# Optimization experiments

Measured on AMD Instinct MI355X. Metric: run time of the kernel, lower is better.

Reference implementation:

```python
import jax, jax.numpy as jnp
import numpy as np

B, S, D_MODEL = 4, 2048, 1024
N_HEADS, D_HEAD = 16, 64
HIDDEN = N_HEADS * D_HEAD
N_PRIM, RANK = 16, 256
CHUNK = 64  # matches CHUNK_SIZE in the torch module


def setup_inputs() -> dict:
    key = jax.random.key(0)
    ks = jax.random.split(key, 16)
    def n(k, shape, scale=0.02):
        return jax.random.normal(k, shape, dtype=jnp.float32) * scale
    return {
        'x': jax.random.normal(ks[0], (B, S, D_MODEL), dtype=jnp.float32),
        'q_U': n(ks[1], (N_PRIM, D_MODEL, RANK)),
        'q_V': n(ks[2], (N_PRIM, RANK, HIDDEN)),
        'k_U': n(ks[3], (N_PRIM, D_MODEL, RANK)),
        'k_V': n(ks[4], (N_PRIM, RANK, HIDDEN)),
        'v_U': n(ks[5], (N_PRIM, D_MODEL, RANK)),
        'v_V': n(ks[6], (N_PRIM, RANK, HIDDEN)),
        'q_logits': jax.random.normal(ks[7], (N_PRIM,), dtype=jnp.float32),
        'k_logits': jax.random.normal(ks[8], (N_PRIM,), dtype=jnp.float32),
        'v_logits': jax.random.normal(ks[9], (N_PRIM,), dtype=jnp.float32),
        'gate_logits': jax.random.normal(ks[10], (N_PRIM,), dtype=jnp.float32),
        'decay_w': n(ks[11], (N_HEADS, D_MODEL), 0.03),
        'decay_b': jnp.full((N_HEADS,), -2.0, dtype=jnp.float32),
        'out_gate_w': n(ks[12], (HIDDEN, D_MODEL), 0.03),
        'out_proj_w': n(ks[13], (D_MODEL, HIDDEN), 0.03),
        'rms_w': jnp.ones((HIDDEN,), dtype=jnp.float32),
        'top_k': 4,
    }


def _bank_topk_fused(x, U, V, logits, top_k):
    """Top-k fused mixture of low-rank primitives: sum_j w_j * (x @ U_j @ V_j)."""
    w = jax.nn.softmax(logits)                      # [P]
    vals, idx = jax.lax.top_k(w, top_k)             # [k], [k]
    vals = vals / jnp.sum(vals)                     # renormalize selected weights
    Us = U[idx]                                     # [k, d_in, rank]
    Vs = V[idx]                                     # [k, rank, d_out]
    h = jnp.einsum('bsd,kdr->bskr', x, Us)          # low-rank bottleneck
    return jnp.einsum('bskr,kro,k->bso', h, Vs, vals)


def _chunked_scan(q, kv, log_decay):
    """Decay-gated linear recurrence via chunked parallel scan (CHUNK=64).
    q, kv: [B,S,H,D]; log_decay: [B,S,H,1]. Returns [B,S,H,D]."""
    b, s, h, d = q.shape
    nc = s // CHUNK
    # [NC, B, C, H, *] chunked layout for lax.scan over chunks
    qc = jnp.moveaxis(q.reshape(b, nc, CHUNK, h, d), 1, 0)
    kvc = jnp.moveaxis(kv.reshape(b, nc, CHUNK, h, d), 1, 0)
    ldc = jnp.moveaxis(log_decay.reshape(b, nc, CHUNK, h, 1), 1, 0)

    def step(state, inp):
        ld, kvs, qs = inp                            # [B,C,H,1], [B,C,H,D], [B,C,H,D]
        cum = jnp.cumsum(ld, axis=1)                 # cumulative log-decay in chunk
        last = cum[:, -1:]
        kv_shifted = kvs * jnp.exp(last - cum)
        new = jnp.exp(cum - last) * jnp.cumsum(kv_shifted, axis=1)
        chunk_states = state[:, None] * jnp.exp(cum) + new   # [B,C,H,D]
        out = qs * chunk_states
        return chunk_states[:, -1], out

    state0 = jnp.zeros((b, h, d), dtype=jnp.float32)
    _, outs = jax.lax.scan(step, state0, (ldc, kvc, qc))     # [NC,B,C,H,D]
    return jnp.moveaxis(outs, 0, 1).reshape(b, s, h, d)


def reference(x, q_U, q_V, k_U, k_V, v_U, v_V,
              q_logits, k_logits, v_logits, gate_logits,
              decay_w, decay_b, out_gate_w, out_proj_w, rms_w, top_k):
    b, s, _ = x.shape
    h, d = decay_w.shape[0], q_V.shape[-1] // decay_w.shape[0]

    q = _bank_topk_fused(x, q_U, q_V, q_logits, top_k).reshape(b, s, h, d)
    k = _bank_topk_fused(x, k_U, k_V, k_logits, top_k).reshape(b, s, h, d)
    v = _bank_topk_fused(x, v_U, v_V, v_logits, top_k).reshape(b, s, h, d)
    # gate shares the V bank (gate = v_bank.forward_topk_fused with gate weights)
    gate = _bank_topk_fused(x, v_U, v_V, gate_logits, top_k).reshape(b, s, h, d)

    log_decay = -jax.nn.softplus(jnp.einsum('bsd,hd->bsh', x, decay_w) + decay_b)[..., None]  # [B,S,H,1]
    kv = jax.nn.sigmoid(gate) * k * v

    out = _chunked_scan(q, kv.astype(jnp.float32), log_decay.astype(jnp.float32))
    out = out.reshape(b, s, h * d)

    # RMSNorm (torch default eps = finfo.eps for fp32)
    eps = jnp.finfo(jnp.float32).eps
    out = out * jax.lax.rsqrt(jnp.mean(out * out, axis=-1, keepdims=True) + eps) * rms_w
    out = out * jax.nn.sigmoid(jnp.einsum('bsd,od->bso', x, out_gate_w))
    return jnp.einsum('bsh,dh->bsd', out, out_proj_w)
```

## Files before the change

kernel.cpp:

```cpp
#include <hip/hip_runtime.h>
#include <hip/hip_bf16.h>

#define TOK 8192
#define SEQ 2048
#define CT  32
#define NC  64

typedef __attribute__((ext_vector_type(8))) short bf16x8;
typedef __attribute__((ext_vector_type(4))) float f32x4;
typedef unsigned short u16;
typedef unsigned int   u32;

__device__ __forceinline__ u16 f2bf(float f) {
    u32 u = __float_as_uint(f);
    u = (u + 0x7FFFu + ((u >> 16) & 1u)) >> 16;
    return (u16)u;
}
__device__ __forceinline__ float b2f(u16 h) { return __uint_as_float(((u32)h) << 16); }
__device__ __forceinline__ float sigf(float z) { return 1.f / (1.f + __expf(-z)); }

__device__ __forceinline__ void topk4(const float* __restrict__ lg, int* idx, float* wv)
{
    float v[16];
    #pragma unroll
    for (int i = 0; i < 16; i++) v[i] = lg[i];
    bool used[16];
    #pragma unroll
    for (int i = 0; i < 16; i++) used[i] = false;
    float val[4];
    #pragma unroll
    for (int k = 0; k < 4; k++) {
        int bi = 0; float bv = -3.0e38f;
        #pragma unroll
        for (int i = 0; i < 16; i++)
            if (!used[i] && v[i] > bv) { bv = v[i]; bi = i; }
        used[bi] = true; idx[k] = bi; val[k] = bv;
    }
    float e[4], s = 0.f;
    #pragma unroll
    for (int k = 0; k < 4; k++) { e[k] = expf(val[k] - val[0]); s += e[k]; }
    #pragma unroll
    for (int k = 0; k < 4; k++) wv[k] = e[k] / s;
}

__global__ __launch_bounds__(256)
void prep(const float* __restrict__ x, const float* __restrict__ ogw,
          const float* __restrict__ opw,
          const float* __restrict__ qU, const float* __restrict__ kU,
          const float* __restrict__ vU,
          const float* __restrict__ qV, const float* __restrict__ kV,
          const float* __restrict__ vV,
          const float* __restrict__ ql, const float* __restrict__ kl,
          const float* __restrict__ vl, const float* __restrict__ gl,
          const float* __restrict__ dw, const float* __restrict__ db,
          u16* __restrict__ xb, u16* __restrict__ ogwb, u16* __restrict__ opwb,
          u16* __restrict__ gU, u16* __restrict__ gVT, float* __restrict__ dec)
{
    const int blk = blockIdx.x;
    const int tid = threadIdx.x;

    if (blk < 10240) {
        const int i = blk * 256 + tid;
        const float* src; u16* dst; int off;
        if (i < 2097152)      { src = x;   dst = xb;   off = i; }
        else if (i < 2359296) { src = ogw; dst = ogwb; off = i - 2097152; }
        else                  { src = opw; dst = opwb; off = i - 2359296; }
        const float4 v = ((const float4*)src)[off];
        __align__(8) u16 t[4] = { f2bf(v.x), f2bf(v.y), f2bf(v.z), f2bf(v.w) };
        ((uint2*)dst)[off] = *(const uint2*)t;
        return;
    }
    if (blk < 12288) {
        const int local = blk - 10240;
        const int z = local >> 8;
        const int bx = local & 15, by = (local >> 4) & 15;
        const int p = z & 3;
        const float* lg = (p == 0) ? ql : (p == 1) ? kl : (p == 2) ? vl : gl;
        int idx[4]; float wsel[4];
        topk4(lg, idx, wsel);

        if (z < 4) {
            const float* V = (p == 0) ? qV : (p == 1) ? kV : vV;
            const int o0 = bx * 64, k0 = by * 64;
            const int s = k0 >> 8, r0 = k0 & 255;
            const float* Vb = V + (size_t)idx[s] * (256 * 1024);
            __shared__ float tile[64][68];
            const int rr = tid >> 4, cc = (tid & 15) << 2;
            #pragma unroll
            for (int i = 0; i < 4; i++) {
                const float4 v = *(const float4*)(Vb + (size_t)(r0 + rr + 16 * i) * 1024 + o0 + cc);
                *(float4*)&tile[rr + 16 * i][cc] = v;
            }
            __syncthreads();
            const int oo = tid >> 4, kk = (tid & 15) << 2;
            u16* out = gVT + (size_t)p * 1048576;
            #pragma unroll
            for (int i = 0; i < 4; i++) {
                __align__(8) u16 t[4];
                #pragma unroll
                for (int j = 0; j < 4; j++) t[j] = f2bf(tile[kk + j][oo + 16 * i]);
                *(uint2*)(out + (size_t)(o0 + oo + 16 * i) * 1024 + k0 + kk) = *(const uint2*)t;
            }
        } else {
            const float* U = (p == 0) ? qU : (p == 1) ? kU : vU;
            const int d0 = bx * 64, k0 = by * 64;
            const int s = k0 >> 8, r0 = k0 & 255;
            const float* Ub = U + (size_t)idx[s] * (1024 * 256);
            const float wq = wsel[s];
            u16* out = gU + (size_t)p * 1048576;
            const int rr = tid >> 4, cc = (tid & 15) << 2;
            #pragma unroll
            for (int i = 0; i < 4; i++) {
                const float4 v = *(const float4*)(Ub + (size_t)(d0 + rr + 16 * i) * 256 + r0 + cc);
                __align__(8) u16 t[4] = { f2bf(v.x * wq), f2bf(v.y * wq),
                                          f2bf(v.z * wq), f2bf(v.w * wq) };
                *(uint2*)(out + (size_t)(d0 + rr + 16 * i) * 1024 + k0 + cc) = *(const uint2*)t;
            }
        }
        return;
    }
    {
        const int tg = blk - 12288;
        const int wave = tid >> 6, lane = tid & 63;
        const int t = tg * 4 + wave;
        const float4* x4 = (const float4*)(x + (size_t)t * 1024);
        float4 xv[4];
        #pragma unroll
        for (int i = 0; i < 4; i++) xv[i] = x4[lane + 64 * i];
        float p[16];
        #pragma unroll
        for (int h = 0; h < 16; h++) {
            const float4* w4 = (const float4*)(dw + (size_t)h * 1024);
            float s = 0.f;
            #pragma unroll
            for (int i = 0; i < 4; i++) {
                const float4 wv = w4[lane + 64 * i];
                s = fmaf(xv[i].x, wv.x, fmaf(xv[i].y, wv.y,
                    fmaf(xv[i].z, wv.z, fmaf(xv[i].w, wv.w, s))));
            }
            p[h] = s;
        }
        #pragma unroll
        for (int off = 32; off > 0; off >>= 1)
            #pragma unroll
            for (int h = 0; h < 16; h++) p[h] += __shfl_xor(p[h], off);
        if (lane == 0) {
            #pragma unroll
            for (int h = 0; h < 16; h++)
                dec[(size_t)t * 16 + h] = 1.f / (1.f + __expf(p[h] + db[h]));
        }
    }
}

__global__ __launch_bounds__(256)
void mfma_gemm64(const u16* __restrict__ Asrc, const u16* __restrict__ Bsrc,
                 u16* __restrict__ Cout)
{
    __shared__ u16 As[64 * 64];
    __shared__ u16 Bs[64 * 64];
    const int z = blockIdx.z;
    const u16* A = Asrc + (size_t)z * 1048576;
    const u16* B = Bsrc + (size_t)z * 1048576;
    u16* C = Cout + (size_t)z * 1048576;
    const int tid = threadIdx.x, lane = tid & 63, wave = tid >> 6;
    const int m0 = blockIdx.y * 64, n0 = blockIdx.x * 64;
    const int wn = wave * 16;

    f32x4 acc[4];
    #pragma unroll
    for (int i = 0; i < 4; i++) acc[i] = (f32x4)0.f;

    for (int k0 = 0; k0 < 1024; k0 += 64) {
        __syncthreads();
        #pragma unroll
        for (int it = 0; it < 2; it++) {
            const int c   = it * 256 + tid;
            const int row = c >> 3, j = c & 7;
            const int g   = j ^ (row & 7);
            const u16* ga = A + (size_t)(m0 + row) * 1024 + k0 + g * 8;
            __builtin_amdgcn_global_load_lds(
                (const __attribute__((address_space(1))) u32*)ga,
                (__attribute__((address_space(3))) u32*)&As[(it * 256 + wave * 64) * 8],
                16, 0, 0);
            const u16* gb = B + (size_t)(n0 + row) * 1024 + k0 + g * 8;
            __builtin_amdgcn_global_load_lds(
                (const __attribute__((address_space(1))) u32*)gb,
                (__attribute__((address_space(3))) u32*)&Bs[(it * 256 + wave * 64) * 8],
                16, 0, 0);
        }
        __syncthreads();
        #pragma unroll
        for (int ks = 0; ks < 2; ks++) {
            const int gk = ks * 4 + (lane >> 4);
            const int rn = wn + (lane & 15);
            const int jb = gk ^ (rn & 7);
            const bf16x8 bfr = *(const bf16x8*)&Bs[rn * 64 + jb * 8];
            #pragma unroll
            for (int mi = 0; mi < 4; mi++) {
                const int rm = mi * 16 + (lane & 15);
                const int ja = gk ^ (rm & 7);
                const bf16x8 af = *(const bf16x8*)&As[rm * 64 + ja * 8];
                acc[mi] = __builtin_amdgcn_mfma_f32_16x16x32_bf16(af, bfr, acc[mi], 0, 0, 0);
            }
        }
    }
    const int col_l = lane & 15, row_l = (lane >> 4) * 4;
    #pragma unroll
    for (int mi = 0; mi < 4; mi++)
        #pragma unroll
        for (int i = 0; i < 4; i++)
            C[(size_t)(m0 + mi * 16 + row_l + i) * 1024 + n0 + wn + col_l] = f2bf(acc[mi][i]);
}

template<int OUTBF>
__global__ __launch_bounds__(256)
void mfma_gemm(const u16* __restrict__ Asrc, const u16* __restrict__ Bt,
               void* __restrict__ Cout, size_t astride, size_t bstride, size_t cstride)
{
    __shared__ u16 As[128 * 64];
    __shared__ u16 Bs[128 * 64];
    const int flat = blockIdx.x + 8 * (blockIdx.y + 64 * blockIdx.z);
    const int xcd = flat & 7;
    const int r   = flat >> 3;
    const int nb = r & 7, mlocal = (r >> 3) & 7, zb = r >> 6;
    const int m0 = (xcd * 8 + mlocal) * 128, n0 = nb * 128;

    const u16* A = Asrc + (size_t)zb * astride;
    const u16* B = Bt   + (size_t)zb * bstride;
    const int tid  = threadIdx.x;
    const int lane = tid & 63, wave = tid >> 6;
    const int wm = (wave >> 1) * 64, wn = (wave & 1) * 64;

    f32x4 acc[4][4];
    #pragma unroll
    for (int i = 0; i < 4; i++)
        #pragma unroll
        for (int j = 0; j < 4; j++) acc[i][j] = (f32x4)0.f;

    for (int k0 = 0; k0 < 1024; k0 += 64) {
        __syncthreads();
        #pragma unroll
        for (int it = 0; it < 4; it++) {
            const int c   = it * 256 + tid;
            const int row = c >> 3, j = c & 7;
            const int g   = j ^ (row & 7);
            const u16* ga = A + (size_t)(m0 + row) * 1024 + k0 + g * 8;
            __builtin_amdgcn_global_load_lds(
                (const __attribute__((address_space(1))) u32*)ga,
                (__attribute__((address_space(3))) u32*)&As[(it * 256 + wave * 64) * 8],
                16, 0, 0);
            const u16* gb = B + (size_t)(n0 + row) * 1024 + k0 + g * 8;
            __builtin_amdgcn_global_load_lds(
                (const __attribute__((address_space(1))) u32*)gb,
                (__attribute__((address_space(3))) u32*)&Bs[(it * 256 + wave * 64) * 8],
                16, 0, 0);
        }
        __syncthreads();
        #pragma unroll
        for (int ks = 0; ks < 2; ks++) {
            bf16x8 af[4], bfr[4];
            const int gk = ks * 4 + (lane >> 4);
            #pragma unroll
            for (int mi = 0; mi < 4; mi++) {
                const int rr  = wm + mi * 16 + (lane & 15);
                const int ja = gk ^ (rr & 7);
                af[mi] = *(const bf16x8*)&As[rr * 64 + ja * 8];
                const int rn = wn + mi * 16 + (lane & 15);
                const int jb = gk ^ (rn & 7);
                bfr[mi] = *(const bf16x8*)&Bs[rn * 64 + jb * 8];
            }
            #pragma unroll
            for (int mi = 0; mi < 4; mi++)
                #pragma unroll
                for (int ni = 0; ni < 4; ni++)
                    acc[mi][ni] = __builtin_amdgcn_mfma_f32_16x16x32_bf16(
                        af[mi], bfr[ni], acc[mi][ni], 0, 0, 0);
        }
    }
    const int col_l = lane & 15, row_l = (lane >> 4) * 4;
    if (OUTBF) {
        u16* C = (u16*)Cout + (size_t)zb * cstride;
        #pragma unroll
        for (int mi = 0; mi < 4; mi++)
            #pragma unroll
            for (int ni = 0; ni < 4; ni++)
                #pragma unroll
                for (int i = 0; i < 4; i++) {
                    const int rw  = m0 + wm + mi * 16 + row_l + i;
                    const int cn = n0 + wn + ni * 16 + col_l;
                    C[(size_t)rw * 1024 + cn] = f2bf(acc[mi][ni][i]);
                }
    } else {
        float* C = (float*)Cout + (size_t)zb * cstride;
        #pragma unroll
        for (int mi = 0; mi < 4; mi++)
            #pragma unroll
            for (int ni = 0; ni < 4; ni++)
                #pragma unroll
                for (int i = 0; i < 4; i++) {
                    const int rw  = m0 + wm + mi * 16 + row_l + i;
                    const int cn = n0 + wn + ni * 16 + col_l;
                    C[(size_t)rw * 1024 + cn] = acc[mi][ni][i];
                }
    }
}

__global__ __launch_bounds__(64)
void scan1(const u16* __restrict__ Kq, const u16* __restrict__ Vq, const u16* __restrict__ Gq,
           const float* __restrict__ dec, u16* __restrict__ kvb,
           float* __restrict__ Lc, float* __restrict__ Pc)
{
    const int c = blockIdx.x & (NC - 1), h = (blockIdx.x >> 6) & 15, b = blockIdx.x >> 10;
    const int d = threadIdx.x;
    const size_t t0 = (size_t)b * SEQ + c * CT;
    const size_t base = t0 * 1024 + h * 64 + d;
    const u16* kp = Kq + base;
    const u16* vp = Vq + base;
    const u16* gp = Gq + base;
    const float* dp = dec + t0 * 16 + h;
    float s = 0.f, P = 1.f;
    #pragma unroll 4
    for (int t = 0; t < CT; t++) {
        const size_t o = (size_t)t * 1024;
        const float a  = dp[t * 16];
        const u16 kq = f2bf(b2f(kp[o]) * b2f(vp[o]) * sigf(b2f(gp[o])));
        kvb[base + o] = kq;
        s = fmaf(a, s, b2f(kq));
        P *= a;
    }
    const int ci = (b * 16 + h) * NC + c;
    Lc[(size_t)ci * 64 + d] = s;
    if (d == 0) Pc[ci] = P;
}

__global__ __launch_bounds__(64)
void scan3(const u16* __restrict__ Qq, const u16* __restrict__ kvb,
           const float* __restrict__ dec,
           const float* __restrict__ Lc, const float* __restrict__ Pc,
           u16* __restrict__ attb)
{
    const int c = blockIdx.x & (NC - 1), h = (blockIdx.x >> 6) & 15, b = blockIdx.x >> 10;
    const int d = threadIdx.x;
    const size_t t0 = (size_t)b * SEQ + c * CT;
    const size_t base = t0 * 1024 + h * 64 + d;
    const u16* qp = Qq + base;
    const u16* kp = kvb + base;
    const float* dp = dec + t0 * 16 + h;

    const int ci0 = (b * 16 + h) * NC;
    float s = 0.f;
    for (int cc = 0; cc < c; cc++)
        s = fmaf(Pc[ci0 + cc], s, Lc[(size_t)(ci0 + cc) * 64 + d]);

    #pragma unroll 4
    for (int t = 0; t < CT; t++) {
        const size_t o = (size_t)t * 1024;
        const float a  = dp[t * 16];
        s = fmaf(a, s, b2f(kp[o]));
        attb[base + o] = f2bf(b2f(qp[o]) * s);
    }
}

__global__ __launch_bounds__(256)
void rms_gate(const u16* __restrict__ attb, const u16* __restrict__ gpre,
              const float* __restrict__ rmsw, u16* __restrict__ o)
{
    const size_t t = blockIdx.x;
    const int tid = threadIdx.x;
    const ushort4 a4 = ((const ushort4*)(attb + t * 1024))[tid];
    const float ax = b2f(a4.x), ay = b2f(a4.y), az = b2f(a4.z), aw = b2f(a4.w);
    float ss = ax*ax + ay*ay + az*az + aw*aw;
    #pragma unroll
    for (int d = 32; d > 0; d >>= 1) ss += __shfl_down(ss, d);
    __shared__ float red[4];
    if ((tid & 63) == 0) red[tid >> 6] = ss;
    __syncthreads();
    const float tot = red[0] + red[1] + red[2] + red[3];
    const float scale = rsqrtf(tot * (1.0f / 1024.0f) + 1.1920929e-7f);
    const ushort4 g4 = ((const ushort4*)(gpre + t * 1024))[tid];
    const float4 w   = ((const float4*)rmsw)[tid];
    __align__(8) u16 r[4];
    r[0] = f2bf(ax * scale * w.x * sigf(b2f(g4.x)));
    r[1] = f2bf(ay * scale * w.y * sigf(b2f(g4.y)));
    r[2] = f2bf(az * scale * w.z * sigf(b2f(g4.z)));
    r[3] = f2bf(aw * scale * w.w * sigf(b2f(g4.w)));
    ((uint2*)(o + t * 1024))[tid] = *(const uint2*)r;
}

extern "C" void kernel_launch(void* const* d_in, const int* in_sizes, int n_in,
                              void* d_out, int out_size, void* d_ws, size_t ws_size,
                              hipStream_t stream)
{
    const float* x    = (const float*)d_in[0];
    const float* qU   = (const float*)d_in[1];
    const float* qV   = (const float*)d_in[2];
    const float* kU   = (const float*)d_in[3];
    const float* kV   = (const float*)d_in[4];
    const float* vU   = (const float*)d_in[5];
    const float* vV   = (const float*)d_in[6];
    const float* ql   = (const float*)d_in[7];
    const float* kl   = (const float*)d_in[8];
    const float* vl   = (const float*)d_in[9];
    const float* gl   = (const float*)d_in[10];
    const float* dw   = (const float*)d_in[11];
    const float* db   = (const float*)d_in[12];
    const float* ogw  = (const float*)d_in[13];
    const float* opw  = (const float*)d_in[14];
    const float* rmsw = (const float*)d_in[15];

    char* w = (char*)d_ws;
    float* dec  = (float*)(w + 0);
    u16*   WT   = (u16*)  (w + 524288);
    u16*   xb   = (u16*)  (w + 11010048);
    u16*   opwb = (u16*)  (w + 27787264);
    u16*   QKVG = (u16*)  (w + 29884416);
    u16*   RMSO = (u16*)  (w + 113770496);
    u16*   ATTb = (u16*)  (w + 130547712);
    u16*   kvb  = (u16*)  (w + 147324928);
    float* Lc   = (float*)(w + 164102144);
    float* Pc   = (float*)(w + 165150720);
    u16*   gU   = QKVG;
    u16*   gVT  = QKVG + 4194304;
    u16*   ogwb = WT + 4 * 1048576;
    u16*   GPRE = QKVG + 4 * 8388608;

    prep<<<14336, 256, 0, stream>>>(x, ogw, opw, qU, kU, vU, qV, kV, vV,
                                    ql, kl, vl, gl, dw, db,
                                    xb, ogwb, opwb, gU, gVT, dec);

    mfma_gemm64<<<dim3(16, 16, 4), 256, 0, stream>>>(gVT, gU, WT);

    mfma_gemm<1><<<dim3(8, 64, 5), 256, 0, stream>>>(xb, WT, QKVG,
                                                     (size_t)0, (size_t)1048576,
                                                     (size_t)8388608);

    scan1<<<4096, 64, 0, stream>>>(QKVG + 8388608, QKVG + 16777216, QKVG + 25165824,
                                   dec, kvb, Lc, Pc);
    scan3<<<4096, 64, 0, stream>>>(QKVG, kvb, dec, Lc, Pc, ATTb);

    rms_gate<<<8192, 256, 0, stream>>>(ATTb, GPRE, rmsw, RMSO);

    mfma_gemm<0><<<dim3(8, 64, 1), 256, 0, stream>>>(RMSO, opwb, (float*)d_out, 0, 0, 0);
}
```

Before: 397.8 us.

## Fuse chunked scan passes into single-pass decoupled look-back kernel

Replaces the two scan kernels with one kernel that computes kv per chunk, publishes chunk aggregates with flags, and does a decoupled look-back to get the prefix state before producing outputs. This removes the bf16 kv intermediate round-trip, a second kernel launch, and the quadratic per-chunk prefix loop in scan3. It adds a flag memset, spin-waiting that depends on block scheduling order, and keeps 64 floats in registers per thread.

```diff
diff --git a/kernel.cpp b/kernel.cpp
--- a/kernel.cpp
+++ b/kernel.cpp
@@ -306,58 +306,67 @@
 }
 
 __global__ __launch_bounds__(64)
-void scan1(const u16* __restrict__ Kq, const u16* __restrict__ Vq, const u16* __restrict__ Gq,
-           const float* __restrict__ dec, u16* __restrict__ kvb,
-           float* __restrict__ Lc, float* __restrict__ Pc)
-{
-    const int c = blockIdx.x & (NC - 1), h = (blockIdx.x >> 6) & 15, b = blockIdx.x >> 10;
+void scan_lb(const u16* __restrict__ Qq, const u16* __restrict__ Kq,
+             const u16* __restrict__ Vq, const u16* __restrict__ Gq,
+             const float* __restrict__ dec,
+             float* __restrict__ Lagg, float* __restrict__ Sincl,
+             float* __restrict__ Pagg, u32* __restrict__ flags,
+             u16* __restrict__ attb)
+{
+    const int ci = blockIdx.x;
+    const int c = ci & (NC - 1), h = (ci >> 6) & 15, b = ci >> 10;
     const int d = threadIdx.x;
     const size_t t0 = (size_t)b * SEQ + c * CT;
     const size_t base = t0 * 1024 + h * 64 + d;
-    const u16* kp = Kq + base;
-    const u16* vp = Vq + base;
-    const u16* gp = Gq + base;
     const float* dp = dec + t0 * 16 + h;
-    float s = 0.f, P = 1.f;
-    #pragma unroll 4
+
+    float kvr[CT], ar[CT];
+    float L = 0.f, P = 1.f;
+    #pragma unroll
     for (int t = 0; t < CT; t++) {
         const size_t o = (size_t)t * 1024;
         const float a  = dp[t * 16];
-        const u16 kq = f2bf(b2f(kp[o]) * b2f(vp[o]) * sigf(b2f(gp[o])));
-        kvb[base + o] = kq;
-        s = fmaf(a, s, b2f(kq));
+        const float kv = b2f(Kq[base + o]) * b2f(Vq[base + o]) * sigf(b2f(Gq[base + o]));
+        ar[t] = a; kvr[t] = kv;
+        L = fmaf(a, L, kv);
         P *= a;
     }
-    const int ci = (b * 16 + h) * NC + c;
-    Lc[(size_t)ci * 64 + d] = s;
-    if (d == 0) Pc[ci] = P;
-}
-
-__global__ __launch_bounds__(64)
-void scan3(const u16* __restrict__ Qq, const u16* __restrict__ kvb,
-           const float* __restrict__ dec,
-           const float* __restrict__ Lc, const float* __restrict__ Pc,
-           u16* __restrict__ attb)
-{
-    const int c = blockIdx.x & (NC - 1), h = (blockIdx.x >> 6) & 15, b = blockIdx.x >> 10;
-    const int d = threadIdx.x;
-    const size_t t0 = (size_t)b * SEQ + c * CT;
-    const size_t base = t0 * 1024 + h * 64 + d;
-    const u16* qp = Qq + base;
-    const u16* kp = kvb + base;
-    const float* dp = dec + t0 * 16 + h;
-
-    const int ci0 = (b * 16 + h) * NC;
-    float s = 0.f;
-    for (int cc = 0; cc < c; cc++)
-        s = fmaf(Pc[ci0 + cc], s, Lc[(size_t)(ci0 + cc) * 64 + d]);
-
-    #pragma unroll 4
+
+    float sprev = 0.f;
+    if (c == 0) {
+        Sincl[(size_t)ci * 64 + d] = L;
+        __threadfence();
+        if (d == 0) atomicExch(&flags[ci], 2u);
+    } else {
+        Lagg[(size_t)ci * 64 + d] = L;
+        if (d == 0) Pagg[ci] = P;
+        __threadfence();
+        if (d == 0) atomicExch(&flags[ci], 1u);
+        float carry = 1.f;
+        int j = ci - 1;
+        while (true) {
+            u32 f;
+            do {
+                f = atomicAdd(&flags[j], 0u);
+                if (f == 0u) __builtin_amdgcn_s_sleep(1);
+            } while (f == 0u);
+            __threadfence();
+            if (f == 2u) { sprev = fmaf(carry, Sincl[(size_t)j * 64 + d], sprev); break; }
+            sprev = fmaf(carry, Lagg[(size_t)j * 64 + d], sprev);
+            carry *= Pagg[j];
+            j--;
+        }
+        Sincl[(size_t)ci * 64 + d] = fmaf(P, sprev, L);
+        __threadfence();
+        if (d == 0) atomicExch(&flags[ci], 2u);
+    }
+
+    float s = sprev;
+    #pragma unroll
     for (int t = 0; t < CT; t++) {
         const size_t o = (size_t)t * 1024;
-        const float a  = dp[t * 16];
-        s = fmaf(a, s, b2f(kp[o]));
-        attb[base + o] = f2bf(b2f(qp[o]) * s);
+        s = fmaf(ar[t], s, kvr[t]);
+        attb[base + o] = f2bf(b2f(Qq[base + o]) * s);
     }
 }
 
@@ -409,20 +418,23 @@
     const float* rmsw = (const float*)d_in[15];
 
     char* w = (char*)d_ws;
-    float* dec  = (float*)(w + 0);
-    u16*   WT   = (u16*)  (w + 524288);
-    u16*   xb   = (u16*)  (w + 11010048);
-    u16*   opwb = (u16*)  (w + 27787264);
-    u16*   QKVG = (u16*)  (w + 29884416);
-    u16*   RMSO = (u16*)  (w + 113770496);
-    u16*   ATTb = (u16*)  (w + 130547712);
-    u16*   kvb  = (u16*)  (w + 147324928);
-    float* Lc   = (float*)(w + 164102144);
-    float* Pc   = (float*)(w + 165150720);
-    u16*   gU   = QKVG;
-    u16*   gVT  = QKVG + 4194304;
-    u16*   ogwb = WT + 4 * 1048576;
-    u16*   GPRE = QKVG + 4 * 8388608;
+    float* dec   = (float*)(w + 0);
+    u16*   WT    = (u16*)  (w + 524288);
+    u16*   xb    = (u16*)  (w + 11010048);
+    u16*   opwb  = (u16*)  (w + 27787264);
+    u16*   QKVG  = (u16*)  (w + 29884416);
+    u16*   RMSO  = (u16*)  (w + 113770496);
+    u16*   ATTb  = (u16*)  (w + 130547712);
+    float* Lagg  = (float*)(w + 147324928);
+    float* Sincl = (float*)(w + 148373504);
+    float* Pagg  = (float*)(w + 149422080);
+    u32*   flags = (u32*)  (w + 149438464);
+    u16*   gU    = QKVG;
+    u16*   gVT   = QKVG + 4194304;
+    u16*   ogwb  = WT + 4 * 1048576;
+    u16*   GPRE  = QKVG + 4 * 8388608;
+
+    hipMemsetAsync(flags, 0, 4096 * sizeof(u32), stream);
 
     prep<<<14336, 256, 0, stream>>>(x, ogw, opw, qU, kU, vU, qV, kV, vV,
                                     ql, kl, vl, gl, dw, db,
@@ -434,9 +446,9 @@
                                                      (size_t)0, (size_t)1048576,
                                                      (size_t)8388608);
 
-    scan1<<<4096, 64, 0, stream>>>(QKVG + 8388608, QKVG + 16777216, QKVG + 25165824,
-                                   dec, kvb, Lc, Pc);
-    scan3<<<4096, 64, 0, stream>>>(QKVG, kvb, dec, Lc, Pc, ATTb);
+    scan_lb<<<4096, 64, 0, stream>>>(QKVG, QKVG + 8388608, QKVG + 16777216,
+                                     QKVG + 25165824, dec,
+                                     Lagg, Sincl, Pagg, flags, ATTb);
 
     rms_gate<<<8192, 256, 0, stream>>>(ATTb, GPRE, rmsw, RMSO);
 
```

Result: slower. 1.306 ms (+228.4%).

## Fuse x bf16 conversion into decay projection, pack scan and RMS work per wave

Applied to the files above, without the earlier changes.

The prep kernel now converts x to bf16 in the same per-token pass that computes the decay projection, so x is read once instead of twice, and the grid shrinks. The scan kernels pack four independent (chunk, head, batch) units into each 256-thread block instead of using 64-thread blocks. RMS-gate now handles one token per wave with a shuffle-only reduction, dropping the shared-memory barrier. These changes aim to cut redundant global reads, launch overhead and synchronisation in small elementwise kernels, at little risk beyond a different block-to-work mapping.

```diff
diff --git a/kernel.cpp b/kernel.cpp
--- a/kernel.cpp
+++ b/kernel.cpp
@@ -59,19 +59,56 @@
     const int blk = blockIdx.x;
     const int tid = threadIdx.x;
 
-    if (blk < 10240) {
-        const int i = blk * 256 + tid;
-        const float* src; u16* dst; int off;
-        if (i < 2097152)      { src = x;   dst = xb;   off = i; }
-        else if (i < 2359296) { src = ogw; dst = ogwb; off = i - 2097152; }
-        else                  { src = opw; dst = opwb; off = i - 2359296; }
+    if (blk < 2048) {
+        const int wave = tid >> 6, lane = tid & 63;
+        const int t = blk * 4 + wave;
+        const float4* x4 = (const float4*)(x + (size_t)t * 1024);
+        float4 xv[4];
+        #pragma unroll
+        for (int i = 0; i < 4; i++) xv[i] = x4[lane + 64 * i];
+        uint2* xrow = (uint2*)(xb + (size_t)t * 1024);
+        #pragma unroll
+        for (int i = 0; i < 4; i++) {
+            __align__(8) u16 tq[4] = { f2bf(xv[i].x), f2bf(xv[i].y),
+                                       f2bf(xv[i].z), f2bf(xv[i].w) };
+            xrow[lane + 64 * i] = *(const uint2*)tq;
+        }
+        float p[16];
+        #pragma unroll
+        for (int h = 0; h < 16; h++) {
+            const float4* w4 = (const float4*)(dw + (size_t)h * 1024);
+            float s = 0.f;
+            #pragma unroll
+            for (int i = 0; i < 4; i++) {
+                const float4 wv = w4[lane + 64 * i];
+                s = fmaf(xv[i].x, wv.x, fmaf(xv[i].y, wv.y,
+                    fmaf(xv[i].z, wv.z, fmaf(xv[i].w, wv.w, s))));
+            }
+            p[h] = s;
+        }
+        #pragma unroll
+        for (int off = 32; off > 0; off >>= 1)
+            #pragma unroll
+            for (int h = 0; h < 16; h++) p[h] += __shfl_xor(p[h], off);
+        if (lane == 0) {
+            #pragma unroll
+            for (int h = 0; h < 16; h++)
+                dec[(size_t)t * 16 + h] = 1.f / (1.f + __expf(p[h] + db[h]));
+        }
+        return;
+    }
+    if (blk < 4096) {
+        const float* src; u16* dst;
+        int off;
+        if (blk < 3072) { src = ogw; dst = ogwb; off = (blk - 2048) * 256 + tid; }
+        else            { src = opw; dst = opwb; off = (blk - 3072) * 256 + tid; }
         const float4 v = ((const float4*)src)[off];
         __align__(8) u16 t[4] = { f2bf(v.x), f2bf(v.y), f2bf(v.z), f2bf(v.w) };
         ((uint2*)dst)[off] = *(const uint2*)t;
         return;
     }
-    if (blk < 12288) {
-        const int local = blk - 10240;
+    {
+        const int local = blk - 4096;
         const int z = local >> 8;
         const int bx = local & 15, by = (local >> 4) & 15;
         const int p = z & 3;
@@ -116,38 +153,6 @@
                                           f2bf(v.z * wq), f2bf(v.w * wq) };
                 *(uint2*)(out + (size_t)(d0 + rr + 16 * i) * 1024 + k0 + cc) = *(const uint2*)t;
             }
-        }
-        return;
-    }
-    {
-        const int tg = blk - 12288;
-        const int wave = tid >> 6, lane = tid & 63;
-        const int t = tg * 4 + wave;
-        const float4* x4 = (const float4*)(x + (size_t)t * 1024);
-        float4 xv[4];
-        #pragma unroll
-        for (int i = 0; i < 4; i++) xv[i] = x4[lane + 64 * i];
-        float p[16];
-        #pragma unroll
-        for (int h = 0; h < 16; h++) {
-            const float4* w4 = (const float4*)(dw + (size_t)h * 1024);
-            float s = 0.f;
-            #pragma unroll
-            for (int i = 0; i < 4; i++) {
-                const float4 wv = w4[lane + 64 * i];
-                s = fmaf(xv[i].x, wv.x, fmaf(xv[i].y, wv.y,
-                    fmaf(xv[i].z, wv.z, fmaf(xv[i].w, wv.w, s))));
-            }
-            p[h] = s;
-        }
-        #pragma unroll
-        for (int off = 32; off > 0; off >>= 1)
-            #pragma unroll
-            for (int h = 0; h < 16; h++) p[h] += __shfl_xor(p[h], off);
-        if (lane == 0) {
-            #pragma unroll
-            for (int h = 0; h < 16; h++)
-                dec[(size_t)t * 16 + h] = 1.f / (1.f + __expf(p[h] + db[h]));
         }
     }
 }
@@ -305,13 +310,14 @@
     }
 }
 
-__global__ __launch_bounds__(64)
+__global__ __launch_bounds__(256)
 void scan1(const u16* __restrict__ Kq, const u16* __restrict__ Vq, const u16* __restrict__ Gq,
            const float* __restrict__ dec, u16* __restrict__ kvb,
            float* __restrict__ Lc, float* __restrict__ Pc)
 {
-    const int c = blockIdx.x & (NC - 1), h = (blockIdx.x >> 6) & 15, b = blockIdx.x >> 10;
-    const int d = threadIdx.x;
+    const int unit = blockIdx.x * 4 + (threadIdx.x >> 6);
+    const int d = threadIdx.x & 63;
+    const int c = unit & (NC - 1), h = (unit >> 6) & 15, b = unit >> 10;
     const size_t t0 = (size_t)b * SEQ + c * CT;
     const size_t base = t0 * 1024 + h * 64 + d;
     const u16* kp = Kq + base;
@@ -333,14 +339,15 @@
     if (d == 0) Pc[ci] = P;
 }
 
-__global__ __launch_bounds__(64)
+__global__ __launch_bounds__(256)
 void scan3(const u16* __restrict__ Qq, const u16* __restrict__ kvb,
            const float* __restrict__ dec,
            const float* __restrict__ Lc, const float* __restrict__ Pc,
            u16* __restrict__ attb)
 {
-    const int c = blockIdx.x & (NC - 1), h = (blockIdx.x >> 6) & 15, b = blockIdx.x >> 10;
-    const int d = threadIdx.x;
+    const int unit = blockIdx.x * 4 + (threadIdx.x >> 6);
+    const int d = threadIdx.x & 63;
+    const int c = unit & (NC - 1), h = (unit >> 6) & 15, b = unit >> 10;
     const size_t t0 = (size_t)b * SEQ + c * CT;
     const size_t base = t0 * 1024 + h * 64 + d;
     const u16* qp = Qq + base;
@@ -365,26 +372,35 @@
 void rms_gate(const u16* __restrict__ attb, const u16* __restrict__ gpre,
               const float* __restrict__ rmsw, u16* __restrict__ o)
 {
-    const size_t t = blockIdx.x;
-    const int tid = threadIdx.x;
-    const ushort4 a4 = ((const ushort4*)(attb + t * 1024))[tid];
-    const float ax = b2f(a4.x), ay = b2f(a4.y), az = b2f(a4.z), aw = b2f(a4.w);
-    float ss = ax*ax + ay*ay + az*az + aw*aw;
-    #pragma unroll
-    for (int d = 32; d > 0; d >>= 1) ss += __shfl_down(ss, d);
-    __shared__ float red[4];
-    if ((tid & 63) == 0) red[tid >> 6] = ss;
-    __syncthreads();
-    const float tot = red[0] + red[1] + red[2] + red[3];
-    const float scale = rsqrtf(tot * (1.0f / 1024.0f) + 1.1920929e-7f);
-    const ushort4 g4 = ((const ushort4*)(gpre + t * 1024))[tid];
-    const float4 w   = ((const float4*)rmsw)[tid];
-    __align__(8) u16 r[4];
-    r[0] = f2bf(ax * scale * w.x * sigf(b2f(g4.x)));
-    r[1] = f2bf(ay * scale * w.y * sigf(b2f(g4.y)));
-    r[2] = f2bf(az * scale * w.z * sigf(b2f(g4.z)));
-    r[3] = f2bf(aw * scale * w.w * sigf(b2f(g4.w)));
-    ((uint2*)(o + t * 1024))[tid] = *(const uint2*)r;
+    const int wave = threadIdx.x >> 6, lane = threadIdx.x & 63;
+    const size_t t = (size_t)blockIdx.x * 4 + wave;
+    const ushort4* ap = (const ushort4*)(attb + t * 1024);
+    ushort4 a4[4];
+    float ss = 0.f;
+    #pragma unroll
+    for (int i = 0; i < 4; i++) {
+        a4[i] = ap[lane + 64 * i];
+        const float ax = b2f(a4[i].x), ay = b2f(a4[i].y);
+        const float az = b2f(a4[i].z), aw = b2f(a4[i].w);
+        ss += ax*ax + ay*ay + az*az + aw*aw;
+    }
+    #pragma unroll
+    for (int off = 32; off > 0; off >>= 1) ss += __shfl_xor(ss, off);
+    const float scale = rsqrtf(ss * (1.0f / 1024.0f) + 1.1920929e-7f);
+    const ushort4* gp = (const ushort4*)(gpre + t * 1024);
+    const float4*  wp = (const float4*)rmsw;
+    uint2* op = (uint2*)(o + t * 1024);
+    #pragma unroll
+    for (int i = 0; i < 4; i++) {
+        const ushort4 g4 = gp[lane + 64 * i];
+        const float4  w  = wp[lane + 64 * i];
+        __align__(8) u16 r[4];
+        r[0] = f2bf(b2f(a4[i].x) * scale * w.x * sigf(b2f(g4.x)));
+        r[1] = f2bf(b2f(a4[i].y) * scale * w.y * sigf(b2f(g4.y)));
+        r[2] = f2bf(b2f(a4[i].z) * scale * w.z * sigf(b2f(g4.z)));
+        r[3] = f2bf(b2f(a4[i].w) * scale * w.w * sigf(b2f(g4.w)));
+        op[lane + 64 * i] = *(const uint2*)r;
+    }
 }
 
 extern "C" void kernel_launch(void* const* d_in, const int* in_sizes, int n_in,
@@ -424,9 +440,9 @@
     u16*   ogwb = WT + 4 * 1048576;
     u16*   GPRE = QKVG + 4 * 8388608;
 
-    prep<<<14336, 256, 0, stream>>>(x, ogw, opw, qU, kU, vU, qV, kV, vV,
-                                    ql, kl, vl, gl, dw, db,
-                                    xb, ogwb, opwb, gU, gVT, dec);
+    prep<<<6144, 256, 0, stream>>>(x, ogw, opw, qU, kU, vU, qV, kV, vV,
+                                   ql, kl, vl, gl, dw, db,
+                                   xb, ogwb, opwb, gU, gVT, dec);
 
     mfma_gemm64<<<dim3(16, 16, 4), 256, 0, stream>>>(gVT, gU, WT);
 
@@ -434,11 +450,11 @@
                                                      (size_t)0, (size_t)1048576,
                                                      (size_t)8388608);
 
-    scan1<<<4096, 64, 0, stream>>>(QKVG + 8388608, QKVG + 16777216, QKVG + 25165824,
-                                   dec, kvb, Lc, Pc);
-    scan3<<<4096, 64, 0, stream>>>(QKVG, kvb, dec, Lc, Pc, ATTb);
-
-    rms_gate<<<8192, 256, 0, stream>>>(ATTb, GPRE, rmsw, RMSO);
+    scan1<<<1024, 256, 0, stream>>>(QKVG + 8388608, QKVG + 16777216, QKVG + 25165824,
+                                    dec, kvb, Lc, Pc);
+    scan3<<<1024, 256, 0, stream>>>(QKVG, kvb, dec, Lc, Pc, ATTb);
+
+    rms_gate<<<2048, 256, 0, stream>>>(ATTb, GPRE, rmsw, RMSO);
 
     mfma_gemm<0><<<dim3(8, 64, 1), 256, 0, stream>>>(RMSO, opwb, (float*)d_out, 0, 0, 0);
 }
```

Measured after the change: 391.9 us (median of 2 runs). Within noise of the previous version (-1.5%).
